# Kernel optimization log

Measured on AMD Instinct MI355X. Metric: run time of the kernel, lower is better.

Reference implementation:

```python
import jax, jax.numpy as jnp
import numpy as np
from jax import lax

ALPHA = 1.0
BETA = 0.001
GAMMA = 0.1
THRESHOLD = 0.5
LOG_CLAMP = -100.0  # torch BCELoss clamps log terms at -100


def setup_inputs() -> dict:
    key = jax.random.key(0)
    k1, k2 = jax.random.split(key)
    B, C, H, W = 256, 2, 192, 256
    inputs = jax.random.uniform(k1, (B, C, H, W), dtype=jnp.float32,
                                minval=1e-4, maxval=1.0 - 1e-4)
    targets = jax.random.uniform(k2, (1, B, C, H, W), dtype=jnp.float32)
    return {"inputs": inputs, "targets": targets}


def _bce(p, t):
    # mean-reduced BCE with torch-style log clamping
    logp = jnp.maximum(jnp.log(p), LOG_CLAMP)
    log1mp = jnp.maximum(jnp.log1p(-p), LOG_CLAMP)
    return -jnp.mean(t * logp + (1.0 - t) * log1mp)


def _dense_penalty(mask):
    # mask: [B, H, W] bool. Faithful to the Python loop:
    # for each column, for consecutive True rows (p, c) with p, c in [0, H-2],
    # add 1/(c-p)^3, except when p == 0 (i_before==0 is falsy in the original).
    B, H, W = mask.shape
    prev0 = jnp.zeros((B, W), dtype=jnp.int32)  # 0 encodes "no previous" (matches bug)

    def step(carry, i):
        prev, acc = carry
        m = mask[:, i, :]  # [B, W]
        dist = (i - prev).astype(jnp.float32)
        add = jnp.where(m & (prev != 0), 1.0 / (dist ** 3), 0.0)
        prev = jnp.where(m, i, prev)
        return (prev, acc + jnp.sum(add)), None

    (_, dense), _ = lax.scan(step, (prev0, jnp.float32(0.0)),
                             jnp.arange(H - 1, dtype=jnp.int32))
    return dense


def reference(inputs, targets):
    t = jnp.squeeze(targets, axis=0)  # [B, 2, H, W]
    loss_bce = ALPHA * _bce(inputs, t)
    # limit_num_cuts: count of channel-0 entries above threshold
    loss_cuts = BETA * jnp.sum(inputs[:, 0] > THRESHOLD).astype(jnp.float32)
    # avoid_dense_predictions on channel 1
    loss_dense = GAMMA * _dense_penalty(inputs[:, 1] > THRESHOLD)
    return loss_bce + loss_cuts + loss_dense
```

## Files before the change

### kernel.cpp

```cpp
#include <hip/hip_runtime.h>
#include <math.h>

#define ALPHA     1.0f
#define BETA      0.001f
#define GAMMA     0.1f
#define THRESH    0.5f
#define LOG_CLAMP -100.0f
#define LN2       0.69314718055994530942f

constexpr int B = 256, C = 2, H = 192, W = 256;
constexpr int HW   = H * W;
constexpr int HW4  = HW / 4;
constexpr long long NTOT = (long long)B * C * H * W;
constexpr int N4   = (int)(NTOT / 4);

constexpr int BCE_BLOCKS   = 2048;
constexpr int PAIRS        = 12;
constexpr int DENSE_BLOCKS = 1024;

typedef float vfloat4 __attribute__((ext_vector_type(4)));

__device__ __forceinline__ float fast_log(float x) {
    return fmaxf(__builtin_amdgcn_logf(x) * LN2, LOG_CLAMP);
}

__device__ __forceinline__ vfloat4 nt_load4(const vfloat4* p) {
    return __builtin_nontemporal_load(p);
}

__device__ __forceinline__ float wave_reduce(float v) {
#pragma unroll
    for (int off = 32; off > 0; off >>= 1)
        v += __shfl_down(v, off, 64);
    return v;
}

__global__ __launch_bounds__(256, 8) void bce_cuts_kernel(
        const vfloat4* __restrict__ p4,
        const vfloat4* __restrict__ t4,
        float2* __restrict__ part) {
    const int base = blockIdx.x * (256 * PAIRS) + threadIdx.x;

    float bce  = 0.0f;
    float cuts = 0.0f;

    vfloat4 pc = nt_load4(&p4[base]);
    vfloat4 tc = nt_load4(&t4[base]);

#pragma unroll
    for (int k = 0; k < PAIRS; ++k) {
        vfloat4 pn, tn;
        if (k + 1 < PAIRS) {
            pn = nt_load4(&p4[base + (k + 1) * 256]);
            tn = nt_load4(&t4[base + (k + 1) * 256]);
        }

        const int f = base + k * 256;
        const int c = (f / HW4) & 1;

#pragma unroll
        for (int e = 0; e < 4; ++e) {
            const float pv = pc[e];
            const float tv = tc[e];
            const float lp = fast_log(pv);
            const float lm = fast_log(1.0f - pv);
            bce += lm + tv * (lp - lm);
            if (c == 0)
                cuts += (pv > THRESH ? 1.0f : 0.0f);
        }

        pc = pn;
        tc = tn;
    }

    __shared__ float sb[4], sc[4];
    float rb = wave_reduce(bce);
    float rc = wave_reduce(cuts);
    const int lane = threadIdx.x & 63;
    const int wid  = threadIdx.x >> 6;
    if (lane == 0) { sb[wid] = rb; sc[wid] = rc; }
    __syncthreads();
    if (threadIdx.x == 0) {
        part[blockIdx.x] = make_float2(sb[0] + sb[1] + sb[2] + sb[3],
                                       sc[0] + sc[1] + sc[2] + sc[3]);
    }
}

__global__ __launch_bounds__(256) void dense_kernel(
        const float* __restrict__ in,
        float* __restrict__ part) {
    const int lane = threadIdx.x & 63;
    const int seg  = threadIdx.x >> 6;
    const int j    = blockIdx.x * 64 + lane;
    const int b    = j >> 8;
    const int w    = j & 255;
    const float* col = in + ((b * 2 + 1) * H) * W + w;
    const int segbase = seg * 48;

    float v[48];
#pragma unroll
    for (int k = 0; k < 48; ++k)
        v[k] = col[(segbase + k) * W];

    int   first = -1, last = -1;
    float sum = 0.0f;
#pragma unroll
    for (int k = 0; k < 48; ++k) {
        const int i = segbase + k;
        const bool m = (v[k] > THRESH) && (i != 0) && (i != 191);
        if (m) {
            if (last >= 0) {
                const float d = (float)(i - last);
                sum += __builtin_amdgcn_rcpf(d * d * d);
            } else {
                first = i;
            }
            last = i;
        }
    }

    __shared__ int   sfirst[256];
    __shared__ int   slast[256];
    __shared__ float ssum[256];
    sfirst[threadIdx.x] = first;
    slast[threadIdx.x]  = last;
    ssum[threadIdx.x]   = sum;
    __syncthreads();

    if (threadIdx.x < 64) {
        int   mlast = -1;
        float msum  = 0.0f;
#pragma unroll
        for (int s = 0; s < 4; ++s) {
            const int idx = s * 64 + threadIdx.x;
            const int f = sfirst[idx];
            if (f >= 0) {
                if (mlast >= 0) {
                    const float d = (float)(f - mlast);
                    msum += __builtin_amdgcn_rcpf(d * d * d);
                }
                msum += ssum[idx];
                mlast = slast[idx];
            }
        }
        float r = wave_reduce(msum);
        if (threadIdx.x == 0)
            part[blockIdx.x] = r;
    }
}

__global__ __launch_bounds__(256) void finalize_kernel(
        const float2* __restrict__ part_bce,
        const float* __restrict__ part_dense,
        float* __restrict__ out) {
    float b = 0.0f, c = 0.0f, d = 0.0f;
    for (int i = threadIdx.x; i < BCE_BLOCKS; i += 256) {
        float2 v = part_bce[i];
        b += v.x;
        c += v.y;
    }
    for (int i = threadIdx.x; i < DENSE_BLOCKS; i += 256)
        d += part_dense[i];

    __shared__ float sb[4], sc[4], sd[4];
    float rb = wave_reduce(b);
    float rc = wave_reduce(c);
    float rd = wave_reduce(d);
    const int lane = threadIdx.x & 63;
    const int wid  = threadIdx.x >> 6;
    if (lane == 0) { sb[wid] = rb; sc[wid] = rc; sd[wid] = rd; }
    __syncthreads();
    if (threadIdx.x == 0) {
        const float bce_sum   = sb[0] + sb[1] + sb[2] + sb[3];
        const float cuts_sum  = sc[0] + sc[1] + sc[2] + sc[3];
        const float dense_sum = sd[0] + sd[1] + sd[2] + sd[3];
        const float bce = -bce_sum / (float)NTOT;
        out[0] = ALPHA * bce + BETA * cuts_sum + GAMMA * dense_sum;
    }
}

extern "C" void kernel_launch(void* const* d_in, const int* in_sizes, int n_in,
                              void* d_out, int out_size, void* d_ws, size_t ws_size,
                              hipStream_t stream) {
    const float* inputs  = (const float*)d_in[0];
    const float* targets = (const float*)d_in[1];
    float* out = (float*)d_out;

    float2* part_bce   = (float2*)d_ws;
    float*  part_dense = (float*)d_ws + 2 * BCE_BLOCKS;

    bce_cuts_kernel<<<BCE_BLOCKS, 256, 0, stream>>>(
        (const vfloat4*)inputs, (const vfloat4*)targets, part_bce);

    dense_kernel<<<DENSE_BLOCKS, 256, 0, stream>>>(inputs, part_dense);

    finalize_kernel<<<1, 256, 0, stream>>>(part_bce, part_dense, out);
}
```

Before: 211.4 us.

## Fuse dense-penalty mask extraction into BCE pass via ballot bitmasks

The dense penalty is now computed from the BCE kernel's own loads of channel 1. Each block's chunk of 48 rows x 256 columns is turned into per-column bitmasks using wave ballots and shared memory. Each column's segment of consecutive pairs is then scored with bit scans, and a small merge kernel combines the four segments per column. This removes the dense kernel's second read of channel 1 from global memory. In exchange the BCE kernel gains shared-memory traffic, a bit-transpose loop and more workspace writes, which may affect occupancy.

```diff
diff --git a/kernel.cpp b/kernel.cpp
--- a/kernel.cpp
+++ b/kernel.cpp
@@ -16,7 +16,8 @@
 
 constexpr int BCE_BLOCKS   = 2048;
 constexpr int PAIRS        = 12;
-constexpr int DENSE_BLOCKS = 1024;
+constexpr int NCOL         = B * W;
+constexpr int MERGE_BLOCKS = 256;
 
 typedef float vfloat4 __attribute__((ext_vector_type(4)));
 
@@ -35,11 +36,23 @@
     return v;
 }
 
-__global__ __launch_bounds__(256, 8) void bce_cuts_kernel(
+__global__ __launch_bounds__(256, 8) void bce_cuts_dense_kernel(
         const vfloat4* __restrict__ p4,
         const vfloat4* __restrict__ t4,
-        float2* __restrict__ part) {
-    const int base = blockIdx.x * (256 * PAIRS) + threadIdx.x;
+        float2* __restrict__ part,
+        float* __restrict__ segsum,
+        short* __restrict__ segfirst,
+        short* __restrict__ seglast) {
+    const int bi   = blockIdx.x;
+    const int base = bi * (256 * PAIRS) + threadIdx.x;
+    const int c    = (bi >> 2) & 1;
+    const int s    = bi & 3;
+    const int bb   = bi >> 3;
+    const int lane = threadIdx.x & 63;
+    const int wid  = threadIdx.x >> 6;
+
+    __shared__ unsigned long long rm[48][4];
+    __shared__ float sb[4], sc[4];
 
     float bce  = 0.0f;
     float cuts = 0.0f;
@@ -55,9 +68,7 @@
             tn = nt_load4(&t4[base + (k + 1) * 256]);
         }
 
-        const int f = base + k * 256;
-        const int c = (f / HW4) & 1;
-
+        bool gt[4];
 #pragma unroll
         for (int e = 0; e < 4; ++e) {
             const float pv = pc[e];
@@ -65,88 +76,99 @@
             const float lp = fast_log(pv);
             const float lm = fast_log(1.0f - pv);
             bce += lm + tv * (lp - lm);
-            if (c == 0)
-                cuts += (pv > THRESH ? 1.0f : 0.0f);
+            gt[e] = pv > THRESH;
+        }
+
+        if (c == 0) {
+            cuts += (gt[0] ? 1.0f : 0.0f) + (gt[1] ? 1.0f : 0.0f)
+                  + (gt[2] ? 1.0f : 0.0f) + (gt[3] ? 1.0f : 0.0f);
+        } else {
+            const unsigned long long m0 = __ballot(gt[0]);
+            const unsigned long long m1 = __ballot(gt[1]);
+            const unsigned long long m2 = __ballot(gt[2]);
+            const unsigned long long m3 = __ballot(gt[3]);
+            if (lane == 0) {
+                const int lr = 4 * k + wid;
+                rm[lr][0] = m0; rm[lr][1] = m1;
+                rm[lr][2] = m2; rm[lr][3] = m3;
+            }
         }
 
         pc = pn;
         tc = tn;
     }
 
-    __shared__ float sb[4], sc[4];
     float rb = wave_reduce(bce);
     float rc = wave_reduce(cuts);
+    if (lane == 0) { sb[wid] = rb; sc[wid] = rc; }
+    __syncthreads();
+
+    if (threadIdx.x == 0)
+        part[bi] = make_float2(sb[0] + sb[1] + sb[2] + sb[3],
+                               sc[0] + sc[1] + sc[2] + sc[3]);
+
+    if (c == 1) {
+        const int w = threadIdx.x;
+        const int e = w & 3;
+        const int l = w >> 2;
+        unsigned long long cm = 0ull;
+#pragma unroll
+        for (int lr = 0; lr < 48; ++lr)
+            cm |= ((rm[lr][e] >> l) & 1ull) << lr;
+        if (s == 0) cm &= ~1ull;
+        if (s == 3) cm &= ~(1ull << 47);
+
+        short first = -1, last = -1;
+        float sum = 0.0f;
+        if (cm) {
+            int i = __builtin_ctzll(cm);
+            first = (short)(48 * s + i);
+            unsigned long long m = cm & (cm - 1);
+            int prev = i;
+            while (m) {
+                const int jj = __builtin_ctzll(m);
+                const float d = (float)(jj - prev);
+                sum += __builtin_amdgcn_rcpf(d * d * d);
+                prev = jj;
+                m &= m - 1;
+            }
+            last = (short)(48 * s + prev);
+        }
+        const int j = bb * 256 + w;
+        segsum  [s * NCOL + j] = sum;
+        segfirst[s * NCOL + j] = first;
+        seglast [s * NCOL + j] = last;
+    }
+}
+
+__global__ __launch_bounds__(256) void dense_merge_kernel(
+        const float* __restrict__ segsum,
+        const short* __restrict__ segfirst,
+        const short* __restrict__ seglast,
+        float* __restrict__ part) {
+    const int j = blockIdx.x * 256 + threadIdx.x;
+    int   mlast = -1;
+    float msum  = 0.0f;
+#pragma unroll
+    for (int s = 0; s < 4; ++s) {
+        const int f = segfirst[s * NCOL + j];
+        if (f >= 0) {
+            if (mlast >= 0) {
+                const float d = (float)(f - mlast);
+                msum += __builtin_amdgcn_rcpf(d * d * d);
+            }
+            msum += segsum[s * NCOL + j];
+            mlast = seglast[s * NCOL + j];
+        }
+    }
+    float r = wave_reduce(msum);
+    __shared__ float sd[4];
     const int lane = threadIdx.x & 63;
     const int wid  = threadIdx.x >> 6;
-    if (lane == 0) { sb[wid] = rb; sc[wid] = rc; }
+    if (lane == 0) sd[wid] = r;
     __syncthreads();
-    if (threadIdx.x == 0) {
-        part[blockIdx.x] = make_float2(sb[0] + sb[1] + sb[2] + sb[3],
-                                       sc[0] + sc[1] + sc[2] + sc[3]);
-    }
-}
-
-__global__ __launch_bounds__(256) void dense_kernel(
-        const float* __restrict__ in,
-        float* __restrict__ part) {
-    const int lane = threadIdx.x & 63;
-    const int seg  = threadIdx.x >> 6;
-    const int j    = blockIdx.x * 64 + lane;
-    const int b    = j >> 8;
-    const int w    = j & 255;
-    const float* col = in + ((b * 2 + 1) * H) * W + w;
-    const int segbase = seg * 48;
-
-    float v[48];
-#pragma unroll
-    for (int k = 0; k < 48; ++k)
-        v[k] = col[(segbase + k) * W];
-
-    int   first = -1, last = -1;
-    float sum = 0.0f;
-#pragma unroll
-    for (int k = 0; k < 48; ++k) {
-        const int i = segbase + k;
-        const bool m = (v[k] > THRESH) && (i != 0) && (i != 191);
-        if (m) {
-            if (last >= 0) {
-                const float d = (float)(i - last);
-                sum += __builtin_amdgcn_rcpf(d * d * d);
-            } else {
-                first = i;
-            }
-            last = i;
-        }
-    }
-
-    __shared__ int   sfirst[256];
-    __shared__ int   slast[256];
-    __shared__ float ssum[256];
-    sfirst[threadIdx.x] = first;
-    slast[threadIdx.x]  = last;
-    ssum[threadIdx.x]   = sum;
-    __syncthreads();
-
-    if (threadIdx.x < 64) {
-        int   mlast = -1;
-        float msum  = 0.0f;
-#pragma unroll
-        for (int s = 0; s < 4; ++s) {
-            const int idx = s * 64 + threadIdx.x;
-            const int f = sfirst[idx];
-            if (f >= 0) {
-                if (mlast >= 0) {
-                    const float d = (float)(f - mlast);
-                    msum += __builtin_amdgcn_rcpf(d * d * d);
-                }
-                msum += ssum[idx];
-                mlast = slast[idx];
-            }
-        }
-        float r = wave_reduce(msum);
-        if (threadIdx.x == 0)
-            part[blockIdx.x] = r;
-    }
+    if (threadIdx.x == 0)
+        part[blockIdx.x] = sd[0] + sd[1] + sd[2] + sd[3];
 }
 
 __global__ __launch_bounds__(256) void finalize_kernel(
@@ -159,7 +181,7 @@
         b += v.x;
         c += v.y;
     }
-    for (int i = threadIdx.x; i < DENSE_BLOCKS; i += 256)
+    for (int i = threadIdx.x; i < MERGE_BLOCKS; i += 256)
         d += part_dense[i];
 
     __shared__ float sb[4], sc[4], sd[4];
@@ -186,13 +208,19 @@
     const float* targets = (const float*)d_in[1];
     float* out = (float*)d_out;
 
-    float2* part_bce   = (float2*)d_ws;
-    float*  part_dense = (float*)d_ws + 2 * BCE_BLOCKS;
-
-    bce_cuts_kernel<<<BCE_BLOCKS, 256, 0, stream>>>(
-        (const vfloat4*)inputs, (const vfloat4*)targets, part_bce);
-
-    dense_kernel<<<DENSE_BLOCKS, 256, 0, stream>>>(inputs, part_dense);
+    float2* part_bce = (float2*)d_ws;
+    char*   p        = (char*)d_ws + BCE_BLOCKS * sizeof(float2);
+    float*  segsum   = (float*)p;  p += 4 * NCOL * sizeof(float);
+    short*  segfirst = (short*)p;  p += 4 * NCOL * sizeof(short);
+    short*  seglast  = (short*)p;  p += 4 * NCOL * sizeof(short);
+    float*  part_dense = (float*)p;
+
+    bce_cuts_dense_kernel<<<BCE_BLOCKS, 256, 0, stream>>>(
+        (const vfloat4*)inputs, (const vfloat4*)targets,
+        part_bce, segsum, segfirst, seglast);
+
+    dense_merge_kernel<<<MERGE_BLOCKS, 256, 0, stream>>>(
+        segsum, segfirst, seglast, part_dense);
 
     finalize_kernel<<<1, 256, 0, stream>>>(part_bce, part_dense, out);
 }
```

New measurement: 236.3 us. 1.12x slower.
